# Kernel tuning notes

Measured on AMD Instinct MI355X. Metric: run time of the kernel, lower is better.

Reference implementation:

```python
import math
import jax, jax.numpy as jnp
import numpy as np

B, S, D = 4, 2048, 1024
L = 2                      # codec_decoder_transformer_lengths entry
H, HD = 8, 128             # n_heads == n_kv_heads (no GQA repeat)
FF = 4096
WINDOW = 16                # sliding window (causal: keys in [i-16, i])
NORM_EPS = 0.01
QK_EPS = 1e-6
SCALE_INIT = 0.1           # layer_id < 18 -> 0.1


def _alibi_slopes(n):
    # n is a power of 2 here (8)
    r = 2.0 ** (-8.0 / n)
    return jnp.array([r ** (i + 1) for i in range(n)], dtype=jnp.float32)


def rms_norm(x, w, eps):
    return x * jax.lax.rsqrt(jnp.mean(x * x, axis=-1, keepdims=True) + eps) * w


def _attn_bias(dtype):
    pos = jnp.arange(S)
    rel = pos[None, :] - pos[:, None]          # [S,S], rel = j - i
    slopes = _alibi_slopes(H).astype(dtype)
    bias = slopes[:, None, None] * rel[None].astype(dtype)   # [H,S,S]
    mask = (rel > 0) | (rel < -WINDOW)         # causal + sliding window
    return jnp.where(mask[None], -jnp.inf, bias)


def setup_inputs() -> dict:
    key = jax.random.key(0)
    ks = jax.random.split(key, 9)
    sd = 0.02
    w = lambda k, shape: jax.random.normal(k, shape, jnp.float32) * sd
    return {
        "x": jax.random.normal(ks[0], (B, S, D), jnp.float32),
        "wq": w(ks[1], (L, D, H * HD)),
        "wk": w(ks[2], (L, D, H * HD)),
        "wv": w(ks[3], (L, D, H * HD)),
        "wo": w(ks[4], (L, H * HD, D)),
        "q_norm_w": jnp.ones((L, H * HD), jnp.float32),
        "k_norm_w": jnp.ones((L, H * HD), jnp.float32),
        "w1": w(ks[5], (L, D, FF)),
        "w2": w(ks[6], (L, FF, D)),
        "w3": w(ks[7], (L, D, FF)),
        "attn_norm_w": jnp.ones((L, D), jnp.float32),
        "ffn_norm_w": jnp.ones((L, D), jnp.float32),
        "attn_scale": jnp.full((L, D), SCALE_INIT, jnp.float32),
        "ffn_scale": jnp.full((L, D), SCALE_INIT, jnp.float32),
    }


def reference(x, wq, wk, wv, wo, q_norm_w, k_norm_w, w1, w2, w3,
              attn_norm_w, ffn_norm_w, attn_scale, ffn_scale):
    bias = _attn_bias(x.dtype)                 # [H,S,S]
    inv_sqrt_d = 1.0 / math.sqrt(HD)

    def block(h, p):
        (lwq, lwk, lwv, lwo, qnw, knw, lw1, lw2, lw3, anw, fnw, asc, fsc) = p
        xn = rms_norm(h, anw, NORM_EPS)
        # qk_norm applied on the flat (H*HD) projection before the head split
        q = rms_norm(xn @ lwq, qnw, QK_EPS).reshape(B, S, H, HD).transpose(0, 2, 1, 3)
        k = rms_norm(xn @ lwk, knw, QK_EPS).reshape(B, S, H, HD).transpose(0, 2, 1, 3)
        v = (xn @ lwv).reshape(B, S, H, HD).transpose(0, 2, 1, 3)
        scores = jnp.einsum('bhqd,bhkd->bhqk', q, k) * inv_sqrt_d + bias[None]
        attn = jax.nn.softmax(scores, axis=-1)
        y = jnp.einsum('bhqk,bhkd->bhqd', attn, v)
        y = y.transpose(0, 2, 1, 3).reshape(B, S, H * HD)
        h = h + asc * (y @ lwo)
        xn = rms_norm(h, fnw, NORM_EPS)
        ff = (jax.nn.silu(xn @ lw1) * (xn @ lw3)) @ lw2
        return h + fsc * ff, None

    out, _ = jax.lax.scan(
        block, x,
        (wq, wk, wv, wo, q_norm_w, k_norm_w, w1, w2, w3,
         attn_norm_w, ffn_norm_w, attn_scale, ffn_scale))
    return out
```

## Files before the change

kernel.cpp:

```cpp
#include <hip/hip_runtime.h>

#define B_ 4
#define S_ 2048
#define D_ 1024
#define H_ 8
#define HD_ 128
#define FF_ 4096
#define R_ (B_*S_)

typedef __attribute__((ext_vector_type(8))) short short8;
typedef __attribute__((ext_vector_type(4))) float f32x4;

__device__ __forceinline__ unsigned short f2bf(float f) {
  unsigned int u = __float_as_uint(f);
  return (unsigned short)((u + 0x7fffu + ((u >> 16) & 1u)) >> 16);
}
__device__ __forceinline__ float bf2f(unsigned short s) {
  return __uint_as_float(((unsigned int)s) << 16);
}

typedef const __attribute__((address_space(1))) unsigned int* gas_p;
typedef __attribute__((address_space(3))) unsigned int* las_p;
__device__ __forceinline__ void gload16(const void* g, void* l) {
  __builtin_amdgcn_global_load_lds((gas_p)g, (las_p)l, 16, 0, 0);
}

__global__ __launch_bounds__(256) void f2bf_t_all(
    const float* __restrict__ wq, const float* __restrict__ wk,
    const float* __restrict__ wv, const float* __restrict__ wo,
    const float* __restrict__ w1, const float* __restrict__ w3,
    const float* __restrict__ w2,
    unsigned short* __restrict__ qkvt, unsigned short* __restrict__ wot,
    unsigned short* __restrict__ w1t, unsigned short* __restrict__ w3t,
    unsigned short* __restrict__ w2t) {
  const int id = blockIdx.x;
  const int l = id >> 14, r = id & 16383;
  const float* src; unsigned short* dst; int Rows, Cols, t2;
  if (r < 4096) {
    Rows = 1024; Cols = 1024; t2 = r & 1023;
    const int wsel = r >> 10;
    if (wsel == 0)      { src = wq + (size_t)l*1048576u; dst = qkvt + (size_t)l*3145728u; }
    else if (wsel == 1) { src = wk + (size_t)l*1048576u; dst = qkvt + (size_t)l*3145728u + 1048576u; }
    else if (wsel == 2) { src = wv + (size_t)l*1048576u; dst = qkvt + (size_t)l*3145728u + 2097152u; }
    else                { src = wo + (size_t)l*1048576u; dst = wot + (size_t)l*1048576u; }
  } else if (r < 12288) {
    Rows = 1024; Cols = 4096; t2 = (r - 4096) & 4095;
    if (r < 8192) { src = w1 + (size_t)l*4194304u; dst = w1t + (size_t)l*4194304u; }
    else          { src = w3 + (size_t)l*4194304u; dst = w3t + (size_t)l*4194304u; }
  } else {
    Rows = 4096; Cols = 1024; t2 = r - 12288;
    src = w2 + (size_t)l*4194304u; dst = w2t + (size_t)l*4194304u;
  }
  const int lgc = (Cols == 4096) ? 7 : 5;
  const int bx = t2 & ((1 << lgc) - 1), by = t2 >> lgc;
  const int r0 = by * 32, c0 = bx * 32;
  __shared__ float tile[32][33];
  const int tx = threadIdx.x & 31, ty = threadIdx.x >> 5;
  #pragma unroll
  for (int j = 0; j < 32; j += 8)
    tile[ty + j][tx] = src[(size_t)(r0 + ty + j) * Cols + c0 + tx];
  __syncthreads();
  #pragma unroll
  for (int j = 0; j < 32; j += 8)
    dst[(size_t)(c0 + ty + j) * Rows + r0 + tx] = f2bf(tile[tx][ty + j]);
}

__global__ __launch_bounds__(256) void rmsnorm_f2b(const float* __restrict__ in,
    const float* __restrict__ w, unsigned short* __restrict__ out, float eps) {
  const int row = blockIdx.x, t = threadIdx.x;
  const float4 xv = *(const float4*)&in[(size_t)row * D_ + t * 4];
  float p = xv.x*xv.x + xv.y*xv.y + xv.z*xv.z + xv.w*xv.w;
  #pragma unroll
  for (int off = 32; off >= 1; off >>= 1) p += __shfl_xor(p, off);
  __shared__ float red[4];
  if ((t & 63) == 0) red[t >> 6] = p;
  __syncthreads();
  float scl = rsqrtf((red[0] + red[1] + red[2] + red[3]) * (1.0f / D_) + eps);
  const float4 wv = *(const float4*)&w[t * 4];
  ((ushort4*)out)[(size_t)row * 256 + t] = make_ushort4(
      f2bf(xv.x*scl*wv.x), f2bf(xv.y*scl*wv.y), f2bf(xv.z*scl*wv.z), f2bf(xv.w*scl*wv.w));
}

__global__ __launch_bounds__(256) void qknorm_k(unsigned short* __restrict__ qkv,
    const float* __restrict__ qw, const float* __restrict__ kw) {
  const int row = blockIdx.x, t = threadIdx.x;
  unsigned short* qp = qkv + (size_t)row * 3072;
  unsigned short* kp = qp + 1024;
  const ushort4 qv = ((const ushort4*)qp)[t];
  const ushort4 kv = ((const ushort4*)kp)[t];
  float q0 = bf2f(qv.x), q1 = bf2f(qv.y), q2 = bf2f(qv.z), q3 = bf2f(qv.w);
  float k0 = bf2f(kv.x), k1 = bf2f(kv.y), k2 = bf2f(kv.z), k3 = bf2f(kv.w);
  float pq = q0*q0 + q1*q1 + q2*q2 + q3*q3;
  float pk = k0*k0 + k1*k1 + k2*k2 + k3*k3;
  #pragma unroll
  for (int off = 32; off >= 1; off >>= 1) { pq += __shfl_xor(pq, off); pk += __shfl_xor(pk, off); }
  __shared__ float redq[4], redk[4];
  if ((t & 63) == 0) { redq[t >> 6] = pq; redk[t >> 6] = pk; }
  __syncthreads();
  float sq = rsqrtf((redq[0]+redq[1]+redq[2]+redq[3]) * (1.0f / D_) + 1e-6f);
  float sk = rsqrtf((redk[0]+redk[1]+redk[2]+redk[3]) * (1.0f / D_) + 1e-6f);
  const float4 qwv = *(const float4*)&qw[t * 4];
  const float4 kwv = *(const float4*)&kw[t * 4];
  ((ushort4*)qp)[t] = make_ushort4(f2bf(q0*sq*qwv.x), f2bf(q1*sq*qwv.y),
                                   f2bf(q2*sq*qwv.z), f2bf(q3*sq*qwv.w));
  ((ushort4*)kp)[t] = make_ushort4(f2bf(k0*sk*kwv.x), f2bf(k1*sk*kwv.y),
                                   f2bf(k2*sk*kwv.z), f2bf(k3*sk*kwv.w));
}

__global__ __launch_bounds__(256) void attn_k(const unsigned short* __restrict__ qkv,
    unsigned short* __restrict__ y) {
  const int lane = threadIdx.x & 63;
  const int wid = (blockIdx.x * 256 + threadIdx.x) >> 6;
  const int i  = wid & (S_ - 1);
  const int bh = wid >> 11;
  const int hh = bh & (H_ - 1);
  const int b  = bh >> 3;
  const float slope = exp2f(-(float)(hh + 1));
  const float inv = 0.088388347648318447f;
  const size_t rowq = ((size_t)(b * S_ + i)) * 3072 + hh * HD_ + lane * 2;
  const ushort2 qv = *(const ushort2*)&qkv[rowq];
  const float qx = bf2f(qv.x), qy = bf2f(qv.y);
  float sc[17];
  #pragma unroll
  for (int jj = 0; jj < 17; ++jj) {
    int j = i - 16 + jj;
    int jc = j < 0 ? 0 : j;
    size_t koff = ((size_t)(b * S_ + jc)) * 3072 + 1024 + hh * HD_ + lane * 2;
    ushort2 kv = *(const ushort2*)&qkv[koff];
    float p = qx * bf2f(kv.x) + qy * bf2f(kv.y);
    p += __shfl_xor(p, 32); p += __shfl_xor(p, 16); p += __shfl_xor(p, 8);
    p += __shfl_xor(p, 4);  p += __shfl_xor(p, 2);  p += __shfl_xor(p, 1);
    sc[jj] = (j >= 0) ? (p * inv + slope * (float)(jj - 16)) : -1e30f;
  }
  float m = sc[0];
  #pragma unroll
  for (int jj = 1; jj < 17; ++jj) m = fmaxf(m, sc[jj]);
  float wsum = 0.f, ax = 0.f, ay = 0.f;
  #pragma unroll
  for (int jj = 0; jj < 17; ++jj) {
    int j = i - 16 + jj;
    int jc = j < 0 ? 0 : j;
    float wgt = expf(sc[jj] - m);
    size_t voff = ((size_t)(b * S_ + jc)) * 3072 + 2048 + hh * HD_ + lane * 2;
    ushort2 vv = *(const ushort2*)&qkv[voff];
    wsum += wgt; ax += wgt * bf2f(vv.x); ay += wgt * bf2f(vv.y);
  }
  float rs = 1.f / wsum;
  size_t yoff = ((size_t)(b * S_ + i)) * 1024 + hh * HD_ + lane * 2;
  *(ushort2*)&y[yoff] = make_ushort2(f2bf(ax * rs), f2bf(ay * rs));
}

__device__ __forceinline__ void stage_tile(const unsigned short* __restrict__ src,
    unsigned short* lds, int rowbase, int K, int k0, int t) {
  #pragma unroll
  for (int it = 0; it < 4; ++it) {
    int g = it * 256 + t;
    int row = g >> 3, slot = g & 7;
    int sc8 = (slot ^ (row & 7)) << 3;
    gload16(&src[(size_t)(rowbase + row) * K + k0 + sc8], &lds[g * 8]);
  }
}

template<int EPI>
__global__ __launch_bounds__(256, 2) void gemm_tn(
    const unsigned short* __restrict__ A, const unsigned short* __restrict__ Bt,
    void* __restrict__ Cout, const float* __restrict__ sc,
    const float* __restrict__ x2, int M, int N, int K) {
  __shared__ __align__(16) unsigned short As[128 * 64];
  __shared__ __align__(16) unsigned short Bs[128 * 64];
  const int t = threadIdx.x;
  const int lane = t & 63, w = t >> 6;
  const int wr = w >> 1, wc = w & 1;
  const int br = blockIdx.y * 128, bc = blockIdx.x * 128;
  const int lr = lane & 15, lk = lane >> 4;
  const int xm = lr & 7;
  f32x4 acc[4][4];
  #pragma unroll
  for (int mi = 0; mi < 4; ++mi)
    #pragma unroll
    for (int ni = 0; ni < 4; ++ni) { f32x4 z = {0.f,0.f,0.f,0.f}; acc[mi][ni] = z; }
  for (int k0 = 0; k0 < K; k0 += 64) {
    stage_tile(A,  As, br, K, k0, t);
    stage_tile(Bt, Bs, bc, K, k0, t);
    __syncthreads();
    #pragma unroll
    for (int kk = 0; kk < 2; ++kk) {
      short8 af[4], bfr[4];
      #pragma unroll
      for (int mi = 0; mi < 4; ++mi)
        af[mi] = *(const short8*)&As[(wr*64 + mi*16 + lr) * 64 + (((kk*4 + lk) ^ xm) << 3)];
      #pragma unroll
      for (int ni = 0; ni < 4; ++ni)
        bfr[ni] = *(const short8*)&Bs[(wc*64 + ni*16 + lr) * 64 + (((kk*4 + lk) ^ xm) << 3)];
      #pragma unroll
      for (int mi = 0; mi < 4; ++mi)
        #pragma unroll
        for (int ni = 0; ni < 4; ++ni)
          acc[mi][ni] = __builtin_amdgcn_mfma_f32_16x16x32_bf16(af[mi], bfr[ni], acc[mi][ni], 0, 0, 0);
    }
    __syncthreads();
  }
  if (EPI == 0) {
    unsigned short* C = (unsigned short*)Cout;
    #pragma unroll
    for (int mi = 0; mi < 4; ++mi)
      #pragma unroll
      for (int ni = 0; ni < 4; ++ni) {
        int row = br + wr * 64 + mi * 16 + lk * 4;
        int col = bc + wc * 64 + ni * 16 + lr;
        #pragma unroll
        for (int r = 0; r < 4; ++r)
          C[(size_t)(row + r) * N + col] = f2bf(acc[mi][ni][r]);
      }
  } else if (EPI == 1) {
    float* hp = (float*)Cout;
    #pragma unroll
    for (int ni = 0; ni < 4; ++ni) {
      int col = bc + wc * 64 + ni * 16 + lr;
      float sv = sc[col];
      #pragma unroll
      for (int mi = 0; mi < 4; ++mi) {
        int row = br + wr * 64 + mi * 16 + lk * 4;
        #pragma unroll
        for (int r = 0; r < 4; ++r)
          hp[(size_t)(row + r) * N + col] += sv * acc[mi][ni][r];
      }
    }
  } else {
    float* hp = (float*)Cout;
    #pragma unroll
    for (int ni = 0; ni < 4; ++ni) {
      int col = bc + wc * 64 + ni * 16 + lr;
      float sv = sc[col];
      #pragma unroll
      for (int mi = 0; mi < 4; ++mi) {
        int row = br + wr * 64 + mi * 16 + lk * 4;
        #pragma unroll
        for (int r = 0; r < 4; ++r)
          hp[(size_t)(row + r) * N + col] = x2[(size_t)(row + r) * N + col] + sv * acc[mi][ni][r];
      }
    }
  }
}

__global__ __launch_bounds__(256, 2) void gemm_w13(
    const unsigned short* __restrict__ A, const unsigned short* __restrict__ B1t,
    const unsigned short* __restrict__ B3t, unsigned short* __restrict__ G,
    int M, int N, int K) {
  __shared__ __align__(16) unsigned short As[128 * 64];
  __shared__ __align__(16) unsigned short B1s[128 * 64];
  __shared__ __align__(16) unsigned short B3s[128 * 64];
  const int t = threadIdx.x;
  const int lane = t & 63, w = t >> 6;
  const int wr = w >> 1, wc = w & 1;
  const int br = blockIdx.y * 128, bc = blockIdx.x * 128;
  const int lr = lane & 15, lk = lane >> 4;
  const int xm = lr & 7;
  f32x4 acc1[4][4], acc3[4][4];
  #pragma unroll
  for (int mi = 0; mi < 4; ++mi)
    #pragma unroll
    for (int ni = 0; ni < 4; ++ni) {
      f32x4 z = {0.f,0.f,0.f,0.f}; acc1[mi][ni] = z; acc3[mi][ni] = z;
    }
  for (int k0 = 0; k0 < K; k0 += 64) {
    stage_tile(A,   As,  br, K, k0, t);
    stage_tile(B1t, B1s, bc, K, k0, t);
    stage_tile(B3t, B3s, bc, K, k0, t);
    __syncthreads();
    #pragma unroll
    for (int kk = 0; kk < 2; ++kk) {
      short8 af[4], b1r[4], b3r[4];
      #pragma unroll
      for (int mi = 0; mi < 4; ++mi)
        af[mi] = *(const short8*)&As[(wr*64 + mi*16 + lr) * 64 + (((kk*4 + lk) ^ xm) << 3)];
      #pragma unroll
      for (int ni = 0; ni < 4; ++ni) {
        b1r[ni] = *(const short8*)&B1s[(wc*64 + ni*16 + lr) * 64 + (((kk*4 + lk) ^ xm) << 3)];
        b3r[ni] = *(const short8*)&B3s[(wc*64 + ni*16 + lr) * 64 + (((kk*4 + lk) ^ xm) << 3)];
      }
      #pragma unroll
      for (int mi = 0; mi < 4; ++mi)
        #pragma unroll
        for (int ni = 0; ni < 4; ++ni) {
          acc1[mi][ni] = __builtin_amdgcn_mfma_f32_16x16x32_bf16(af[mi], b1r[ni], acc1[mi][ni], 0, 0, 0);
          acc3[mi][ni] = __builtin_amdgcn_mfma_f32_16x16x32_bf16(af[mi], b3r[ni], acc3[mi][ni], 0, 0, 0);
        }
    }
    __syncthreads();
  }
  #pragma unroll
  for (int mi = 0; mi < 4; ++mi)
    #pragma unroll
    for (int ni = 0; ni < 4; ++ni) {
      int row = br + wr * 64 + mi * 16 + lk * 4;
      int col = bc + wc * 64 + ni * 16 + lr;
      #pragma unroll
      for (int r = 0; r < 4; ++r) {
        float a1 = acc1[mi][ni][r], a3 = acc3[mi][ni][r];
        G[(size_t)(row + r) * N + col] = f2bf(a1 / (1.f + expf(-a1)) * a3);
      }
    }
}

extern "C" void kernel_launch(void* const* d_in, const int* in_sizes, int n_in,
                              void* d_out, int out_size, void* d_ws, size_t ws_size,
                              hipStream_t stream) {
  const float* x    = (const float*)d_in[0];
  const float* wq   = (const float*)d_in[1];
  const float* wk   = (const float*)d_in[2];
  const float* wv   = (const float*)d_in[3];
  const float* wo   = (const float*)d_in[4];
  const float* qnw  = (const float*)d_in[5];
  const float* knw  = (const float*)d_in[6];
  const float* w1   = (const float*)d_in[7];
  const float* w2   = (const float*)d_in[8];
  const float* w3   = (const float*)d_in[9];
  const float* anw  = (const float*)d_in[10];
  const float* fnw  = (const float*)d_in[11];
  const float* asc  = (const float*)d_in[12];
  const float* fsc  = (const float*)d_in[13];

  const size_t MB = 1024 * 1024;
  if (ws_size < 144 * MB) return;

  float* h = (float*)d_out;
  char* ws = (char*)d_ws;
  unsigned short* qkvt = (unsigned short*)ws;
  unsigned short* wot  = qkvt + 2u * 3145728u;
  unsigned short* w1t  = wot  + 2u * 1048576u;
  unsigned short* w3t  = w1t  + 2u * 4194304u;
  unsigned short* w2t  = w3t  + 2u * 4194304u;
  unsigned short* xn   = (unsigned short*)(ws + 64 * MB);
  unsigned short* qkv  = (unsigned short*)(ws + 80 * MB);
  unsigned short* gate = qkv;

  f2bf_t_all<<<32768, 256, 0, stream>>>(wq, wk, wv, wo, w1, w3, w2,
                                        qkvt, wot, w1t, w3t, w2t);

  for (int l = 0; l < 2; ++l) {
    rmsnorm_f2b<<<R_, 256, 0, stream>>>(l == 0 ? x : h, anw + l * D_, xn, 0.01f);
    gemm_tn<0><<<dim3(24, 64), 256, 0, stream>>>(xn, qkvt + (size_t)l*3145728u, qkv,
                                                 nullptr, nullptr, R_, 3072, 1024);
    qknorm_k<<<R_, 256, 0, stream>>>(qkv, qnw + l * 1024, knw + l * 1024);
    attn_k<<<R_ * H_ / 4, 256, 0, stream>>>(qkv, xn);
    if (l == 0)
      gemm_tn<2><<<dim3(8, 64), 256, 0, stream>>>(xn, wot, h, asc, x, R_, 1024, 1024);
    else
      gemm_tn<1><<<dim3(8, 64), 256, 0, stream>>>(xn, wot + 1048576u, h, asc + D_,
                                                  nullptr, R_, 1024, 1024);
    rmsnorm_f2b<<<R_, 256, 0, stream>>>(h, fnw + l * D_, xn, 0.01f);
    gemm_w13<<<dim3(32, 64), 256, 0, stream>>>(xn, w1t + (size_t)l*4194304u,
                                               w3t + (size_t)l*4194304u, gate, R_, 4096, 1024);
    gemm_tn<1><<<dim3(8, 64), 256, 0, stream>>>(gate, w2t + (size_t)l*4194304u, h,
                                                fsc + l * D_, nullptr, R_, 1024, 4096);
  }
}
```

Before: 897.2 us.

## Add 256x256 eight-wave pipelined GEMM for QKV and interleaved W1/W3 projections

Adds a new 512-thread GEMM kernel with 256x256 tiles, a double-buffered LDS pipeline using direct global-to-LDS loads, explicit waitcnt/barrier scheduling and raised wave priority around MFMA blocks. The QKV projection and the FFN up-projection now use it. W1 and W3 are interleaved in 16-column groups at conversion time so that one GEMM with N=8192 yields paired gate/up accumulators for the fused SiLU epilogue. The aim is higher MFMA utilisation and more data reuse than the older 128x128 kernels, at the cost of one block per CU and hand-tuned synchronisation that could be fragile.

```diff
diff --git a/kernel.cpp b/kernel.cpp
--- a/kernel.cpp
+++ b/kernel.cpp
@@ -31,11 +31,11 @@
     const float* __restrict__ w1, const float* __restrict__ w3,
     const float* __restrict__ w2,
     unsigned short* __restrict__ qkvt, unsigned short* __restrict__ wot,
-    unsigned short* __restrict__ w1t, unsigned short* __restrict__ w3t,
-    unsigned short* __restrict__ w2t) {
+    unsigned short* __restrict__ w13t, unsigned short* __restrict__ w2t) {
   const int id = blockIdx.x;
   const int l = id >> 14, r = id & 16383;
   const float* src; unsigned short* dst; int Rows, Cols, t2;
+  bool inter = false, sel3 = false;
   if (r < 4096) {
     Rows = 1024; Cols = 1024; t2 = r & 1023;
     const int wsel = r >> 10;
@@ -45,8 +45,9 @@
     else                { src = wo + (size_t)l*1048576u; dst = wot + (size_t)l*1048576u; }
   } else if (r < 12288) {
     Rows = 1024; Cols = 4096; t2 = (r - 4096) & 4095;
-    if (r < 8192) { src = w1 + (size_t)l*4194304u; dst = w1t + (size_t)l*4194304u; }
-    else          { src = w3 + (size_t)l*4194304u; dst = w3t + (size_t)l*4194304u; }
+    inter = true; sel3 = (r >= 8192);
+    src = (sel3 ? w3 : w1) + (size_t)l*4194304u;
+    dst = w13t + (size_t)l*8388608u;
   } else {
     Rows = 4096; Cols = 1024; t2 = r - 12288;
     src = w2 + (size_t)l*4194304u; dst = w2t + (size_t)l*4194304u;
@@ -61,8 +62,11 @@
     tile[ty + j][tx] = src[(size_t)(r0 + ty + j) * Cols + c0 + tx];
   __syncthreads();
   #pragma unroll
-  for (int j = 0; j < 32; j += 8)
-    dst[(size_t)(c0 + ty + j) * Rows + r0 + tx] = f2bf(tile[tx][ty + j]);
+  for (int j = 0; j < 32; j += 8) {
+    int c = c0 + ty + j;
+    int drow = inter ? (((c >> 4) << 5) + (sel3 ? 16 : 0) + (c & 15)) : c;
+    dst[(size_t)drow * Rows + r0 + tx] = f2bf(tile[tx][ty + j]);
+  }
 }
 
 __global__ __launch_bounds__(256) void rmsnorm_f2b(const float* __restrict__ in,
@@ -150,6 +154,183 @@
   *(ushort2*)&y[yoff] = make_ushort2(f2bf(ax * rs), f2bf(ay * rs));
 }
 
+template<int EPI>
+__global__ __launch_bounds__(512, 1) void gemm8p(
+    const unsigned short* __restrict__ A, const unsigned short* __restrict__ Bt,
+    unsigned short* __restrict__ Cout, int M, int N, int K) {
+  __shared__ __align__(16) unsigned short lds[65536];
+  const int t = threadIdx.x;
+  const int lane = t & 63, w = t >> 6;
+  const int wm = w >> 2, wn = w & 3;
+  const int lr = lane & 15, lk = lane >> 4;
+  const int xm = lr & 7;
+  const int br = blockIdx.y << 8, bc = blockIdx.x << 8;
+
+  const unsigned short* Ab = A + (size_t)br * K;
+  const unsigned short* Bb = Bt + (size_t)bc * K;
+
+  auto stageA = [&](int ldsoff, int u, int k0) {
+    #pragma unroll
+    for (int j = 0; j < 2; ++j) {
+      int idx = t + (j << 9);
+      int gr = idx >> 3, slot = idx & 7;
+      int row = ((gr & 63) | ((gr >> 6) << 7)) + (u << 6);
+      gload16(Ab + (size_t)row * K + k0 + ((slot ^ (row & 7)) << 3),
+              &lds[ldsoff + row * 64 + slot * 8]);
+    }
+  };
+  auto stageB = [&](int ldsoff, int half, int k0) {
+    #pragma unroll
+    for (int j = 0; j < 2; ++j) {
+      int idx = t + (j << 9);
+      int row = (idx >> 3) + (half << 7);
+      int slot = idx & 7;
+      gload16(Bb + (size_t)row * K + k0 + ((slot ^ (row & 7)) << 3),
+              &lds[ldsoff + row * 64 + slot * 8]);
+    }
+  };
+
+  f32x4 acc[8][4];
+  #pragma unroll
+  for (int mi = 0; mi < 8; ++mi)
+    #pragma unroll
+    for (int ni = 0; ni < 4; ++ni) { f32x4 z = {0.f,0.f,0.f,0.f}; acc[mi][ni] = z; }
+
+  short8 af[2][4], bn[2][2];
+  auto rdA = [&](int boff, int mh) {
+    #pragma unroll
+    for (int ks = 0; ks < 2; ++ks)
+      #pragma unroll
+      for (int mf = 0; mf < 4; ++mf)
+        af[ks][mf] = *(const short8*)&lds[boff + (wm*128 + (mh*4+mf)*16 + lr)*64
+                                          + (((ks*4+lk)^xm)<<3)];
+  };
+  auto rdB = [&](int boff, int nh) {
+    #pragma unroll
+    for (int ks = 0; ks < 2; ++ks)
+      #pragma unroll
+      for (int nf = 0; nf < 2; ++nf)
+        bn[ks][nf] = *(const short8*)&lds[boff + 16384 + (wn*64 + (nh*2+nf)*16 + lr)*64
+                                          + (((ks*4+lk)^xm)<<3)];
+  };
+  auto mmaQ = [&](int mh, int nh) {
+    __builtin_amdgcn_s_setprio(1);
+    #pragma unroll
+    for (int mf = 0; mf < 4; ++mf)
+      #pragma unroll
+      for (int nf = 0; nf < 2; ++nf)
+        #pragma unroll
+        for (int ks = 0; ks < 2; ++ks)
+          acc[mh*4+mf][nh*2+nf] = __builtin_amdgcn_mfma_f32_16x16x32_bf16(
+              af[ks][mf], bn[ks][nf], acc[mh*4+mf][nh*2+nf], 0, 0, 0);
+    __builtin_amdgcn_s_setprio(0);
+  };
+
+  const int NT = K >> 6;
+  stageA(0, 0, 0); stageA(0, 1, 0);
+  stageB(16384, 0, 0); stageB(16384, 1, 0);
+  stageA(32768, 0, 64); stageA(32768, 1, 64);
+  asm volatile("s_waitcnt vmcnt(4)" ::: "memory");
+  __builtin_amdgcn_s_barrier();
+
+  const int NI = NT >> 1;
+  #pragma unroll 1
+  for (int kt = 0; kt < NI; ++kt) {
+    const int k1 = ((kt<<1)+1) << 6;
+    const int t2 = (kt<<1)+2;
+    const bool has = (t2 < NT);
+    const int k2 = has ? (t2 << 6) : 0;
+    const int k3 = has ? ((t2+1) << 6) : 0;
+
+    rdA(0, 0); rdB(0, 0);
+    stageB(49152, 0, k1); stageB(49152, 1, k1);
+    asm volatile("s_waitcnt lgkmcnt(8)" ::: "memory");
+    __builtin_amdgcn_s_barrier();
+    asm volatile("s_waitcnt lgkmcnt(0)" ::: "memory");
+    __builtin_amdgcn_sched_barrier(0);
+    mmaQ(0, 0);
+    __builtin_amdgcn_s_barrier();
+    rdB(0, 1);
+    if (has) stageA(0, 0, k2);
+    __builtin_amdgcn_s_barrier();
+    asm volatile("s_waitcnt lgkmcnt(0)" ::: "memory");
+    __builtin_amdgcn_sched_barrier(0);
+    mmaQ(0, 1);
+    __builtin_amdgcn_s_barrier();
+    rdA(0, 1);
+    __builtin_amdgcn_s_barrier();
+    asm volatile("s_waitcnt lgkmcnt(0)" ::: "memory");
+    __builtin_amdgcn_sched_barrier(0);
+    mmaQ(1, 1);
+    __builtin_amdgcn_s_barrier();
+    rdB(0, 0);
+    if (has) { stageA(0, 1, k2);
+               asm volatile("s_waitcnt vmcnt(4)" ::: "memory"); }
+    else     { asm volatile("s_waitcnt vmcnt(0)" ::: "memory"); }
+    __builtin_amdgcn_s_barrier();
+    asm volatile("s_waitcnt lgkmcnt(0)" ::: "memory");
+    __builtin_amdgcn_sched_barrier(0);
+    mmaQ(1, 0);
+    __builtin_amdgcn_s_barrier();
+    rdA(32768, 0); rdB(32768, 0);
+    if (has) { stageB(16384, 0, k2); stageB(16384, 1, k2); }
+    asm volatile("s_waitcnt lgkmcnt(8)" ::: "memory");
+    __builtin_amdgcn_s_barrier();
+    asm volatile("s_waitcnt lgkmcnt(0)" ::: "memory");
+    __builtin_amdgcn_sched_barrier(0);
+    mmaQ(0, 0);
+    __builtin_amdgcn_s_barrier();
+    rdB(32768, 1);
+    if (has) stageA(32768, 0, k3);
+    __builtin_amdgcn_s_barrier();
+    asm volatile("s_waitcnt lgkmcnt(0)" ::: "memory");
+    __builtin_amdgcn_sched_barrier(0);
+    mmaQ(0, 1);
+    __builtin_amdgcn_s_barrier();
+    rdA(32768, 1);
+    __builtin_amdgcn_s_barrier();
+    asm volatile("s_waitcnt lgkmcnt(0)" ::: "memory");
+    __builtin_amdgcn_sched_barrier(0);
+    mmaQ(1, 1);
+    __builtin_amdgcn_s_barrier();
+    rdB(32768, 0);
+    if (has) stageA(32768, 1, k3);
+    asm volatile("s_waitcnt vmcnt(4)" ::: "memory");
+    __builtin_amdgcn_s_barrier();
+    asm volatile("s_waitcnt lgkmcnt(0)" ::: "memory");
+    __builtin_amdgcn_sched_barrier(0);
+    mmaQ(1, 0);
+    __builtin_amdgcn_s_barrier();
+  }
+
+  if (EPI == 0) {
+    #pragma unroll
+    for (int mf = 0; mf < 8; ++mf)
+      #pragma unroll
+      for (int nf = 0; nf < 4; ++nf) {
+        int row = br + wm*128 + mf*16 + lk*4;
+        int col = bc + wn*64 + nf*16 + lr;
+        #pragma unroll
+        for (int r = 0; r < 4; ++r)
+          Cout[(size_t)(row + r) * N + col] = f2bf(acc[mf][nf][r]);
+      }
+  } else {
+    const int NG = N >> 1;
+    #pragma unroll
+    for (int mf = 0; mf < 8; ++mf)
+      #pragma unroll
+      for (int pr = 0; pr < 2; ++pr) {
+        int row = br + wm*128 + mf*16 + lk*4;
+        int gcol = (bc >> 1) + wn*32 + pr*16 + lr;
+        #pragma unroll
+        for (int r = 0; r < 4; ++r) {
+          float a1 = acc[mf][2*pr][r], a3 = acc[mf][2*pr+1][r];
+          Cout[(size_t)(row + r) * NG + gcol] = f2bf(a1 / (1.f + expf(-a1)) * a3);
+        }
+      }
+  }
+}
+
 __device__ __forceinline__ void stage_tile(const unsigned short* __restrict__ src,
     unsigned short* lds, int rowbase, int K, int k0, int t) {
   #pragma unroll
@@ -200,107 +381,23 @@
     }
     __syncthreads();
   }
-  if (EPI == 0) {
-    unsigned short* C = (unsigned short*)Cout;
-    #pragma unroll
-    for (int mi = 0; mi < 4; ++mi)
-      #pragma unroll
-      for (int ni = 0; ni < 4; ++ni) {
-        int row = br + wr * 64 + mi * 16 + lk * 4;
-        int col = bc + wc * 64 + ni * 16 + lr;
-        #pragma unroll
-        for (int r = 0; r < 4; ++r)
-          C[(size_t)(row + r) * N + col] = f2bf(acc[mi][ni][r]);
-      }
-  } else if (EPI == 1) {
-    float* hp = (float*)Cout;
-    #pragma unroll
-    for (int ni = 0; ni < 4; ++ni) {
-      int col = bc + wc * 64 + ni * 16 + lr;
-      float sv = sc[col];
-      #pragma unroll
-      for (int mi = 0; mi < 4; ++mi) {
-        int row = br + wr * 64 + mi * 16 + lk * 4;
-        #pragma unroll
-        for (int r = 0; r < 4; ++r)
+  float* hp = (float*)Cout;
+  #pragma unroll
+  for (int ni = 0; ni < 4; ++ni) {
+    int col = bc + wc * 64 + ni * 16 + lr;
+    float sv = sc[col];
+    #pragma unroll
+    for (int mi = 0; mi < 4; ++mi) {
+      int row = br + wr * 64 + mi * 16 + lk * 4;
+      #pragma unroll
+      for (int r = 0; r < 4; ++r) {
+        if (EPI == 1)
           hp[(size_t)(row + r) * N + col] += sv * acc[mi][ni][r];
-      }
-    }
-  } else {
-    float* hp = (float*)Cout;
-    #pragma unroll
-    for (int ni = 0; ni < 4; ++ni) {
-      int col = bc + wc * 64 + ni * 16 + lr;
-      float sv = sc[col];
-      #pragma unroll
-      for (int mi = 0; mi < 4; ++mi) {
-        int row = br + wr * 64 + mi * 16 + lk * 4;
-        #pragma unroll
-        for (int r = 0; r < 4; ++r)
+        else
           hp[(size_t)(row + r) * N + col] = x2[(size_t)(row + r) * N + col] + sv * acc[mi][ni][r];
       }
     }
   }
-}
-
-__global__ __launch_bounds__(256, 2) void gemm_w13(
-    const unsigned short* __restrict__ A, const unsigned short* __restrict__ B1t,
-    const unsigned short* __restrict__ B3t, unsigned short* __restrict__ G,
-    int M, int N, int K) {
-  __shared__ __align__(16) unsigned short As[128 * 64];
-  __shared__ __align__(16) unsigned short B1s[128 * 64];
-  __shared__ __align__(16) unsigned short B3s[128 * 64];
-  const int t = threadIdx.x;
-  const int lane = t & 63, w = t >> 6;
-  const int wr = w >> 1, wc = w & 1;
-  const int br = blockIdx.y * 128, bc = blockIdx.x * 128;
-  const int lr = lane & 15, lk = lane >> 4;
-  const int xm = lr & 7;
-  f32x4 acc1[4][4], acc3[4][4];
-  #pragma unroll
-  for (int mi = 0; mi < 4; ++mi)
-    #pragma unroll
-    for (int ni = 0; ni < 4; ++ni) {
-      f32x4 z = {0.f,0.f,0.f,0.f}; acc1[mi][ni] = z; acc3[mi][ni] = z;
-    }
-  for (int k0 = 0; k0 < K; k0 += 64) {
-    stage_tile(A,   As,  br, K, k0, t);
-    stage_tile(B1t, B1s, bc, K, k0, t);
-    stage_tile(B3t, B3s, bc, K, k0, t);
-    __syncthreads();
-    #pragma unroll
-    for (int kk = 0; kk < 2; ++kk) {
-      short8 af[4], b1r[4], b3r[4];
-      #pragma unroll
-      for (int mi = 0; mi < 4; ++mi)
-        af[mi] = *(const short8*)&As[(wr*64 + mi*16 + lr) * 64 + (((kk*4 + lk) ^ xm) << 3)];
-      #pragma unroll
-      for (int ni = 0; ni < 4; ++ni) {
-        b1r[ni] = *(const short8*)&B1s[(wc*64 + ni*16 + lr) * 64 + (((kk*4 + lk) ^ xm) << 3)];
-        b3r[ni] = *(const short8*)&B3s[(wc*64 + ni*16 + lr) * 64 + (((kk*4 + lk) ^ xm) << 3)];
-      }
-      #pragma unroll
-      for (int mi = 0; mi < 4; ++mi)
-        #pragma unroll
-        for (int ni = 0; ni < 4; ++ni) {
-          acc1[mi][ni] = __builtin_amdgcn_mfma_f32_16x16x32_bf16(af[mi], b1r[ni], acc1[mi][ni], 0, 0, 0);
-          acc3[mi][ni] = __builtin_amdgcn_mfma_f32_16x16x32_bf16(af[mi], b3r[ni], acc3[mi][ni], 0, 0, 0);
-        }
-    }
-    __syncthreads();
-  }
-  #pragma unroll
-  for (int mi = 0; mi < 4; ++mi)
-    #pragma unroll
-    for (int ni = 0; ni < 4; ++ni) {
-      int row = br + wr * 64 + mi * 16 + lk * 4;
-      int col = bc + wc * 64 + ni * 16 + lr;
-      #pragma unroll
-      for (int r = 0; r < 4; ++r) {
-        float a1 = acc1[mi][ni][r], a3 = acc3[mi][ni][r];
-        G[(size_t)(row + r) * N + col] = f2bf(a1 / (1.f + expf(-a1)) * a3);
-      }
-    }
 }
 
 extern "C" void kernel_launch(void* const* d_in, const int* in_sizes, int n_in,
@@ -328,20 +425,19 @@
   char* ws = (char*)d_ws;
   unsigned short* qkvt = (unsigned short*)ws;
   unsigned short* wot  = qkvt + 2u * 3145728u;
-  unsigned short* w1t  = wot  + 2u * 1048576u;
-  unsigned short* w3t  = w1t  + 2u * 4194304u;
-  unsigned short* w2t  = w3t  + 2u * 4194304u;
+  unsigned short* w13t = wot  + 2u * 1048576u;
+  unsigned short* w2t  = w13t + 2u * 8388608u;
   unsigned short* xn   = (unsigned short*)(ws + 64 * MB);
   unsigned short* qkv  = (unsigned short*)(ws + 80 * MB);
   unsigned short* gate = qkv;
 
   f2bf_t_all<<<32768, 256, 0, stream>>>(wq, wk, wv, wo, w1, w3, w2,
-                                        qkvt, wot, w1t, w3t, w2t);
+                                        qkvt, wot, w13t, w2t);
 
   for (int l = 0; l < 2; ++l) {
     rmsnorm_f2b<<<R_, 256, 0, stream>>>(l == 0 ? x : h, anw + l * D_, xn, 0.01f);
-    gemm_tn<0><<<dim3(24, 64), 256, 0, stream>>>(xn, qkvt + (size_t)l*3145728u, qkv,
-                                                 nullptr, nullptr, R_, 3072, 1024);
+    gemm8p<0><<<dim3(12, 32), 512, 0, stream>>>(xn, qkvt + (size_t)l*3145728u, qkv,
+                                                R_, 3072, 1024);
     qknorm_k<<<R_, 256, 0, stream>>>(qkv, qnw + l * 1024, knw + l * 1024);
     attn_k<<<R_ * H_ / 4, 256, 0, stream>>>(qkv, xn);
     if (l == 0)
@@ -350,8 +446,8 @@
       gemm_tn<1><<<dim3(8, 64), 256, 0, stream>>>(xn, wot + 1048576u, h, asc + D_,
                                                   nullptr, R_, 1024, 1024);
     rmsnorm_f2b<<<R_, 256, 0, stream>>>(h, fnw + l * D_, xn, 0.01f);
-    gemm_w13<<<dim3(32, 64), 256, 0, stream>>>(xn, w1t + (size_t)l*4194304u,
-                                               w3t + (size_t)l*4194304u, gate, R_, 4096, 1024);
+    gemm8p<1><<<dim3(32, 32), 512, 0, stream>>>(xn, w13t + (size_t)l*8388608u, gate,
+                                                R_, 8192, 1024);
     gemm_tn<1><<<dim3(8, 64), 256, 0, stream>>>(gate, w2t + (size_t)l*4194304u, h,
                                                 fsc + l * D_, nullptr, R_, 1024, 4096);
   }
```

Result: slower. 943.5 us (+5.1%).

## Fuse QK RMS-norm into QKV GEMM epilogue and attention kernel

Applied to the files above, without the earlier changes.

Drops the separate qknorm kernel. The QKV GEMM epilogue accumulates per-row sum of squares for the q and k columns into a float buffer with atomics, and the buffer is zeroed by the preceding rmsnorm kernel. The attention kernel applies the norm weights and rsqrt scales on the fly, removing one read-modify-write pass over q and k. In exchange it adds atomic traffic in the GEMM epilogue and extra per-key scale loads in attention.

```diff
diff --git a/kernel.cpp b/kernel.cpp
--- a/kernel.cpp
+++ b/kernel.cpp
@@ -66,8 +66,10 @@
 }
 
 __global__ __launch_bounds__(256) void rmsnorm_f2b(const float* __restrict__ in,
-    const float* __restrict__ w, unsigned short* __restrict__ out, float eps) {
+    const float* __restrict__ w, unsigned short* __restrict__ out, float eps,
+    float* __restrict__ qksc) {
   const int row = blockIdx.x, t = threadIdx.x;
+  if (qksc && t == 0) { qksc[row] = 0.f; qksc[row + 8192] = 0.f; }
   const float4 xv = *(const float4*)&in[(size_t)row * D_ + t * 4];
   float p = xv.x*xv.x + xv.y*xv.y + xv.z*xv.z + xv.w*xv.w;
   #pragma unroll
@@ -81,34 +83,9 @@
       f2bf(xv.x*scl*wv.x), f2bf(xv.y*scl*wv.y), f2bf(xv.z*scl*wv.z), f2bf(xv.w*scl*wv.w));
 }
 
-__global__ __launch_bounds__(256) void qknorm_k(unsigned short* __restrict__ qkv,
+__global__ __launch_bounds__(256) void attn_k(const unsigned short* __restrict__ qkv,
+    unsigned short* __restrict__ y, const float* __restrict__ qksc,
     const float* __restrict__ qw, const float* __restrict__ kw) {
-  const int row = blockIdx.x, t = threadIdx.x;
-  unsigned short* qp = qkv + (size_t)row * 3072;
-  unsigned short* kp = qp + 1024;
-  const ushort4 qv = ((const ushort4*)qp)[t];
-  const ushort4 kv = ((const ushort4*)kp)[t];
-  float q0 = bf2f(qv.x), q1 = bf2f(qv.y), q2 = bf2f(qv.z), q3 = bf2f(qv.w);
-  float k0 = bf2f(kv.x), k1 = bf2f(kv.y), k2 = bf2f(kv.z), k3 = bf2f(kv.w);
-  float pq = q0*q0 + q1*q1 + q2*q2 + q3*q3;
-  float pk = k0*k0 + k1*k1 + k2*k2 + k3*k3;
-  #pragma unroll
-  for (int off = 32; off >= 1; off >>= 1) { pq += __shfl_xor(pq, off); pk += __shfl_xor(pk, off); }
-  __shared__ float redq[4], redk[4];
-  if ((t & 63) == 0) { redq[t >> 6] = pq; redk[t >> 6] = pk; }
-  __syncthreads();
-  float sq = rsqrtf((redq[0]+redq[1]+redq[2]+redq[3]) * (1.0f / D_) + 1e-6f);
-  float sk = rsqrtf((redk[0]+redk[1]+redk[2]+redk[3]) * (1.0f / D_) + 1e-6f);
-  const float4 qwv = *(const float4*)&qw[t * 4];
-  const float4 kwv = *(const float4*)&kw[t * 4];
-  ((ushort4*)qp)[t] = make_ushort4(f2bf(q0*sq*qwv.x), f2bf(q1*sq*qwv.y),
-                                   f2bf(q2*sq*qwv.z), f2bf(q3*sq*qwv.w));
-  ((ushort4*)kp)[t] = make_ushort4(f2bf(k0*sk*kwv.x), f2bf(k1*sk*kwv.y),
-                                   f2bf(k2*sk*kwv.z), f2bf(k3*sk*kwv.w));
-}
-
-__global__ __launch_bounds__(256) void attn_k(const unsigned short* __restrict__ qkv,
-    unsigned short* __restrict__ y) {
   const int lane = threadIdx.x & 63;
   const int wid = (blockIdx.x * 256 + threadIdx.x) >> 6;
   const int i  = wid & (S_ - 1);
@@ -117,20 +94,26 @@
   const int b  = bh >> 3;
   const float slope = exp2f(-(float)(hh + 1));
   const float inv = 0.088388347648318447f;
-  const size_t rowq = ((size_t)(b * S_ + i)) * 3072 + hh * HD_ + lane * 2;
+  const int row_i = b * S_ + i;
+  const size_t rowq = (size_t)row_i * 3072 + hh * HD_ + lane * 2;
   const ushort2 qv = *(const ushort2*)&qkv[rowq];
-  const float qx = bf2f(qv.x), qy = bf2f(qv.y);
+  const float2 qwv = *(const float2*)&qw[hh * HD_ + lane * 2];
+  const float2 kwv = *(const float2*)&kw[hh * HD_ + lane * 2];
+  const float sq = rsqrtf(qksc[row_i] * (1.0f / 1024.0f) + 1e-6f);
+  const float qx = bf2f(qv.x) * qwv.x, qy = bf2f(qv.y) * qwv.y;
   float sc[17];
   #pragma unroll
   for (int jj = 0; jj < 17; ++jj) {
     int j = i - 16 + jj;
     int jc = j < 0 ? 0 : j;
-    size_t koff = ((size_t)(b * S_ + jc)) * 3072 + 1024 + hh * HD_ + lane * 2;
+    int row_j = b * S_ + jc;
+    size_t koff = (size_t)row_j * 3072 + 1024 + hh * HD_ + lane * 2;
     ushort2 kv = *(const ushort2*)&qkv[koff];
-    float p = qx * bf2f(kv.x) + qy * bf2f(kv.y);
+    float p = qx * (bf2f(kv.x) * kwv.x) + qy * (bf2f(kv.y) * kwv.y);
     p += __shfl_xor(p, 32); p += __shfl_xor(p, 16); p += __shfl_xor(p, 8);
     p += __shfl_xor(p, 4);  p += __shfl_xor(p, 2);  p += __shfl_xor(p, 1);
-    sc[jj] = (j >= 0) ? (p * inv + slope * (float)(jj - 16)) : -1e30f;
+    float sk = rsqrtf(qksc[8192 + row_j] * (1.0f / 1024.0f) + 1e-6f);
+    sc[jj] = (j >= 0) ? (p * sq * sk * inv + slope * (float)(jj - 16)) : -1e30f;
   }
   float m = sc[0];
   #pragma unroll
@@ -200,7 +183,7 @@
     }
     __syncthreads();
   }
-  if (EPI == 0) {
+  if (EPI == 0 || EPI == 3) {
     unsigned short* C = (unsigned short*)Cout;
     #pragma unroll
     for (int mi = 0; mi < 4; ++mi)
@@ -212,6 +195,20 @@
         for (int r = 0; r < 4; ++r)
           C[(size_t)(row + r) * N + col] = f2bf(acc[mi][ni][r]);
       }
+    if (EPI == 3 && bc < 2048) {
+      float* sbuf = (float*)sc + (bc < 1024 ? 0 : 8192);
+      #pragma unroll
+      for (int mi = 0; mi < 4; ++mi)
+        #pragma unroll
+        for (int r = 0; r < 4; ++r) {
+          float prt = 0.f;
+          #pragma unroll
+          for (int ni = 0; ni < 4; ++ni) { float v = acc[mi][ni][r]; prt += v * v; }
+          prt += __shfl_xor(prt, 1); prt += __shfl_xor(prt, 2);
+          prt += __shfl_xor(prt, 4); prt += __shfl_xor(prt, 8);
+          if (lr == 0) atomicAdd(&sbuf[br + wr * 64 + mi * 16 + lk * 4 + r], prt);
+        }
+    }
   } else if (EPI == 1) {
     float* hp = (float*)Cout;
     #pragma unroll
@@ -334,22 +331,23 @@
   unsigned short* xn   = (unsigned short*)(ws + 64 * MB);
   unsigned short* qkv  = (unsigned short*)(ws + 80 * MB);
   unsigned short* gate = qkv;
+  float* qksc = (float*)(ws + 143 * MB);
 
   f2bf_t_all<<<32768, 256, 0, stream>>>(wq, wk, wv, wo, w1, w3, w2,
                                         qkvt, wot, w1t, w3t, w2t);
 
   for (int l = 0; l < 2; ++l) {
-    rmsnorm_f2b<<<R_, 256, 0, stream>>>(l == 0 ? x : h, anw + l * D_, xn, 0.01f);
-    gemm_tn<0><<<dim3(24, 64), 256, 0, stream>>>(xn, qkvt + (size_t)l*3145728u, qkv,
-                                                 nullptr, nullptr, R_, 3072, 1024);
-    qknorm_k<<<R_, 256, 0, stream>>>(qkv, qnw + l * 1024, knw + l * 1024);
-    attn_k<<<R_ * H_ / 4, 256, 0, stream>>>(qkv, xn);
+    rmsnorm_f2b<<<R_, 256, 0, stream>>>(l == 0 ? x : h, anw + l * D_, xn, 0.01f, qksc);
+    gemm_tn<3><<<dim3(24, 64), 256, 0, stream>>>(xn, qkvt + (size_t)l*3145728u, qkv,
+                                                 qksc, nullptr, R_, 3072, 1024);
+    attn_k<<<R_ * H_ / 4, 256, 0, stream>>>(qkv, xn, qksc,
+                                            qnw + l * 1024, knw + l * 1024);
     if (l == 0)
       gemm_tn<2><<<dim3(8, 64), 256, 0, stream>>>(xn, wot, h, asc, x, R_, 1024, 1024);
     else
       gemm_tn<1><<<dim3(8, 64), 256, 0, stream>>>(xn, wot + 1048576u, h, asc + D_,
                                                   nullptr, R_, 1024, 1024);
-    rmsnorm_f2b<<<R_, 256, 0, stream>>>(h, fnw + l * D_, xn, 0.01f);
+    rmsnorm_f2b<<<R_, 256, 0, stream>>>(h, fnw + l * D_, xn, 0.01f, nullptr);
     gemm_w13<<<dim3(32, 64), 256, 0, stream>>>(xn, w1t + (size_t)l*4194304u,
                                                w3t + (size_t)l*4194304u, gate, R_, 4096, 1024);
     gemm_tn<1><<<dim3(8, 64), 256, 0, stream>>>(gate, w2t + (size_t)l*4194304u, h,
```

Measured after the change: 944.8 us. +5.3%, slower.
